# Kernel optimization log

Hardware: AMD Instinct MI355X
Metric: run time of the kernel (lower is better)

## Reference

```python
import jax, jax.numpy as jnp
import numpy as np

T, B = 384, 128
IN_DIM, HID, OUT_DIM = 512, 1024, 512


def _lstm_step(h, c, x_t, Wx, Wh, b):
    # x_t: [B, D], h/c: [B, H]; gates order: i, f, g, o
    gates = x_t @ Wx + h @ Wh + b  # [B, 4H]
    i, f, g, o = jnp.split(gates, 4, axis=-1)
    c_new = jax.nn.sigmoid(f) * c + jax.nn.sigmoid(i) * jnp.tanh(g)
    h_new = jax.nn.sigmoid(o) * jnp.tanh(c_new)
    return h_new, c_new


def setup_inputs() -> dict:
    key = jax.random.key(0)
    ks = jax.random.split(key, 9)
    s_in = 1.0 / np.sqrt(IN_DIM)
    s_h = 1.0 / np.sqrt(HID)
    s_o = 1.0 / np.sqrt(OUT_DIM)
    return {
        "x": jax.random.normal(ks[0], (T, B, IN_DIM), dtype=jnp.float32),
        "hidden_state": jnp.zeros((1, B, HID), dtype=jnp.float32),
        "cell_state": jnp.zeros((1, B, HID), dtype=jnp.float32),
        "enc_Wx": jax.random.normal(ks[1], (IN_DIM, 4 * HID), dtype=jnp.float32) * s_in,
        "enc_Wh": jax.random.normal(ks[2], (HID, 4 * HID), dtype=jnp.float32) * s_h,
        "enc_b": jnp.zeros((4 * HID,), dtype=jnp.float32),
        "dec_Wx": jax.random.normal(ks[3], (OUT_DIM, 4 * HID), dtype=jnp.float32) * s_o,
        "dec_Wh": jax.random.normal(ks[4], (HID, 4 * HID), dtype=jnp.float32) * s_h,
        "dec_b": jnp.zeros((4 * HID,), dtype=jnp.float32),
        "fc_W": jax.random.normal(ks[5], (HID, OUT_DIM), dtype=jnp.float32) * s_h,
        "fc_b": jnp.zeros((OUT_DIM,), dtype=jnp.float32),
    }


def reference(x, hidden_state, cell_state, enc_Wx, enc_Wh, enc_b,
              dec_Wx, dec_Wh, dec_b, fc_W, fc_b):
    # ---- encoder: run LSTM over T steps, keep only final hidden state ----
    h0, c0 = hidden_state[0], cell_state[0]  # [B, H]

    def enc_step(carry, x_t):
        h, c = carry
        h, c = _lstm_step(h, c, x_t, enc_Wx, enc_Wh, enc_b)
        return (h, c), None

    (h_enc, _), _ = jax.lax.scan(enc_step, (h0, c0), x)

    y0 = jnp.zeros((B, OUT_DIM), dtype=x.dtype)
    c_dec0 = jnp.zeros((B, HID), dtype=x.dtype)

    def dec_step(carry, _):
        y, h, c = carry
        h, c = _lstm_step(h, c, y, dec_Wx, dec_Wh, dec_b)
        y = jax.nn.softmax(h @ fc_W + fc_b, axis=-1)  # softmax over dim=2
        return (y, h, c), y

    _, output = jax.lax.scan(dec_step, (y0, h_enc, c_dec0), None, length=T)
    return output  # [T, B, OUT_DIM]
```

## Files before the change

### kernel.cpp

```cpp
#include <hip/hip_runtime.h>


#define TS 384

typedef __attribute__((ext_vector_type(8))) short bf16x8;
typedef __attribute__((ext_vector_type(4))) float f32x4;

#define WS_XR 4096u
#define XR_SLOT 262144u
#define WS_HP (WS_XR + 4u*XR_SLOT)
#define HP_BUF 524288u
#define WS_FPN (WS_HP + 2u*HP_BUF)
#define WS_TOTAL (WS_FPN + 2097152u)

__device__ __forceinline__ unsigned short bf16r(float v) {
  unsigned u = __float_as_uint(v);
  u += 0x7FFFu + ((u >> 16) & 1u);
  return (unsigned short)(u >> 16);
}
__device__ __forceinline__ float bf2f(unsigned short h) {
  return __uint_as_float(((unsigned)h) << 16);
}
__device__ __forceinline__ void split2(float v, short& hi, short& lo) {
  unsigned short h = bf16r(v);
  float r = v - bf2f(h);
  hi = (short)h; lo = (short)bf16r(r);
}
__device__ __forceinline__ float sigm(float v)  { return 1.0f / (1.0f + __expf(-v)); }
__device__ __forceinline__ float tanhfa(float v){ return 1.0f - 2.0f / (__expf(2.0f*v) + 1.0f); }

__device__ __forceinline__ void st_u64(short* p, unsigned long long v) {
  __hip_atomic_store((unsigned long long*)p, v, __ATOMIC_RELAXED, __HIP_MEMORY_SCOPE_AGENT);
}
__device__ __forceinline__ void st_f32(float* p, float v) {
  __hip_atomic_store(p, v, __ATOMIC_RELAXED, __HIP_MEMORY_SCOPE_AGENT);
}
__device__ __forceinline__ float ld_f32(const float* p) {
  return __hip_atomic_load(p, __ATOMIC_RELAXED, __HIP_MEMORY_SCOPE_AGENT);
}
__device__ __forceinline__ unsigned ldc(const unsigned* p) {
  return __hip_atomic_load(p, __ATOMIC_RELAXED, __HIP_MEMORY_SCOPE_AGENT);
}

__device__ __forceinline__ void arrive(unsigned* line) {
  asm volatile("s_waitcnt vmcnt(0)" ::: "memory");
  __syncthreads();
  if (threadIdx.x == 0)
    __hip_atomic_fetch_add(line, 1u, __ATOMIC_RELAXED, __HIP_MEMORY_SCOPE_AGENT);
}
__device__ __forceinline__ void wait4(const unsigned* base, unsigned target,
                                      bool fence, int* sDead) {
  if (threadIdx.x == 0) {
    unsigned spins = 0;
    for (;;) {
      unsigned c0 = ldc(base), c1 = ldc(base + 64);
      unsigned c2 = ldc(base + 128), c3 = ldc(base + 192);
      if (c0 >= target && c1 >= target && c2 >= target && c3 >= target) break;
      __builtin_amdgcn_s_sleep(1);
      if (++spins > (1u << 19)) { *sDead = 1; break; }
    }
    if (fence) __builtin_amdgcn_fence(__ATOMIC_ACQUIRE, "agent");
  }
  __syncthreads();
}
__device__ __forceinline__ void wait1(const unsigned* line, unsigned target,
                                      int* sDead) {
  if (threadIdx.x == 0) {
    unsigned spins = 0;
    while (ldc(line) < target) {
      __builtin_amdgcn_s_sleep(1);
      if (++spins > (1u << 19)) { *sDead = 1; break; }
    }
  }
  __syncthreads();
}

__device__ void load_gate_weights(const float* __restrict__ Wx, const float* __restrict__ Wh,
                                  int p, short* sBh, short* sBl) {
  for (int idx = threadIdx.x; idx < 24576; idx += 1024) {
    int j = idx & 7, l = (idx >> 3) & 63, kb = idx >> 9;
    int k = kb * 32 + ((l >> 4) << 3) + j;
    int c = l & 15;
    int gcol = (c >> 2) * 1024 + p * 4 + (c & 3);
    float wv = (k < 512) ? Wx[(size_t)k * 4096 + gcol]
                         : Wh[(size_t)(k - 512) * 4096 + gcol];
    short hi, lo; split2(wv, hi, lo);
    sBh[idx] = hi; sBl[idx] = lo;
  }
}
__device__ void load_fc_weights(const float* __restrict__ fcW, int kg, int cg,
                                short* sFh, short* sFl) {
  for (int idx = threadIdx.x; idx < 4096; idx += 1024) {
    int j = idx & 7, l = (idx >> 3) & 63, kb = idx >> 9;
    int unit = kg * 256 + kb * 32 + ((l >> 4) << 3) + j;
    int col = cg * 16 + (l & 15);
    short hi, lo; split2(fcW[(size_t)unit * 512 + col], hi, lo);
    sFh[idx] = hi; sFl[idx] = lo;
  }
}

__device__ __forceinline__ void gg(const short* AHs, const short* ALs,
    const short* BHs, const short* BLs, int mt, int l,
    int kbA0, int kbB0, int nkb, f32x4* acc)
{
  const bf16x8* AH = (const bf16x8*)AHs;
  const bf16x8* AL = (const bf16x8*)ALs;
  const bf16x8* BH = (const bf16x8*)BHs;
  const bf16x8* BL = (const bf16x8*)BLs;
  #pragma unroll 2
  for (int i = 0; i < nkb; i += 2) {
    int ka = kbA0 + i, kb = kbB0 + i;
    bf16x8 ah0 = AH[(ka * 8 + mt) * 64 + l];
    bf16x8 al0 = AL[(ka * 8 + mt) * 64 + l];
    bf16x8 bh0 = BH[kb * 64 + l];
    bf16x8 bl0 = BL[kb * 64 + l];
    bf16x8 ah1 = AH[((ka + 1) * 8 + mt) * 64 + l];
    bf16x8 al1 = AL[((ka + 1) * 8 + mt) * 64 + l];
    bf16x8 bh1 = BH[(kb + 1) * 64 + l];
    bf16x8 bl1 = BL[(kb + 1) * 64 + l];
    acc[0] = __builtin_amdgcn_mfma_f32_16x16x32_bf16(ah0, bh0, acc[0], 0, 0, 0);
    acc[1] = __builtin_amdgcn_mfma_f32_16x16x32_bf16(ah0, bl0, acc[1], 0, 0, 0);
    acc[2] = __builtin_amdgcn_mfma_f32_16x16x32_bf16(al0, bh0, acc[2], 0, 0, 0);
    acc[3] = __builtin_amdgcn_mfma_f32_16x16x32_bf16(ah1, bh1, acc[3], 0, 0, 0);
    acc[4] = __builtin_amdgcn_mfma_f32_16x16x32_bf16(ah1, bl1, acc[4], 0, 0, 0);
    acc[5] = __builtin_amdgcn_mfma_f32_16x16x32_bf16(al1, bh1, acc[5], 0, 0, 0);
  }
}
__device__ __forceinline__ void gg_finish(f32x4* acc, int kh, int mt, int l,
                                          float* LDSgate) {
  f32x4 s = (acc[0] + acc[3]) + ((acc[1] + acc[4]) + (acc[2] + acc[5]));
  const int col = l & 15, r0 = mt * 16 + ((l >> 4) << 2);
  float* plane = LDSgate + kh * 2176;
  #pragma unroll
  for (int j = 0; j < 4; ++j) plane[(r0 + j) * 17 + col] = s[j];
}

__device__ __forceinline__ void conv_x(const float* __restrict__ xsrc,
                                       short* dstH, short* dstL, int p, int t) {
  if (t < 32) {
    int g = p * 32 + t;
    int l = g & 63, mt = (g >> 6) & 7, kb = g >> 9;
    int row = mt * 16 + (l & 15), k = kb * 32 + ((l >> 4) << 3);
    const float* xs = xsrc + (size_t)row * 512 + k;
    unsigned long long h64[2] = {0, 0}, l64[2] = {0, 0};
    #pragma unroll
    for (int j = 0; j < 8; ++j) {
      short hi, lo; split2(xs[j], hi, lo);
      h64[j >> 2] |= (unsigned long long)(unsigned short)hi << ((j & 3) * 16);
      l64[j >> 2] |= (unsigned long long)(unsigned short)lo << ((j & 3) * 16);
    }
    int off = g * 8;
    st_u64(dstH + off, h64[0]); st_u64(dstH + off + 4, h64[1]);
    st_u64(dstL + off, l64[0]); st_u64(dstL + off + 4, l64[1]);
  }
}

__global__ void __launch_bounds__(1024, 1)
lstm4(const float* __restrict__ x, const float* __restrict__ h0p,
      const float* __restrict__ c0p, const float* __restrict__ eWx,
      const float* __restrict__ eWh, const float* __restrict__ eb,
      const float* __restrict__ dWx, const float* __restrict__ dWh,
      const float* __restrict__ db, const float* __restrict__ fcW,
      const float* __restrict__ fcb, float* __restrict__ out,
      char* __restrict__ ws)
{
  __shared__ __align__(16) short sBh[24576], sBl[24576];
  __shared__ __align__(16) short sFh[4096], sFl[4096];
  __shared__ float LDSgate[2 * 2176];
  __shared__ unsigned hsplit[512];
  __shared__ float ybuf[512];
  __shared__ float red[16];
  __shared__ int sDead;

  const int p = blockIdx.x, t = threadIdx.x;
  const int w = t >> 6, l = t & 63;
  const int mt = w & 7, kh = w >> 3;
  if (t == 0) sDead = 0;

  unsigned* hln = (unsigned*)ws;
  unsigned* yln = (unsigned*)(ws + 1024);
  unsigned* fln = (unsigned*)(ws + 2048);
  unsigned* my_hline = hln + (p >> 6) * 64;

  short* xrH[4]; short* xrL[4];
  #pragma unroll
  for (int s4 = 0; s4 < 4; ++s4) {
    xrH[s4] = (short*)(ws + WS_XR + s4 * XR_SLOT);
    xrL[s4] = (short*)(ws + WS_XR + s4 * XR_SLOT + 131072u);
  }
  short* hpH[2]; short* hpL[2];
  #pragma unroll
  for (int b2 = 0; b2 < 2; ++b2) {
    hpH[b2] = (short*)(ws + WS_HP + b2 * HP_BUF);
    hpL[b2] = (short*)(ws + WS_HP + b2 * HP_BUF + 262144u);
  }
  float* fp = (float*)(ws + WS_FPN);

  const int row_pw = t & 127, u_pw = (t >> 7) & 3;

  load_gate_weights(eWx, eWh, p, sBh, sBl);
  conv_x(x, xrH[0], xrL[0], p, t);
  conv_x(x + 65536, xrH[1], xrL[1], p, t);
  if (t < 64) {
    int hg = p * 64 + t;
    int ll = hg & 63, mtt = (hg >> 6) & 7, hk = hg >> 9;
    int row = mtt * 16 + (ll & 15), k = hk * 32 + ((ll >> 4) << 3);
    const float* hs = h0p + (size_t)row * 1024 + k;
    unsigned long long h64[2] = {0, 0}, l64[2] = {0, 0};
    #pragma unroll
    for (int j = 0; j < 8; ++j) {
      short hi, lo; split2(hs[j], hi, lo);
      h64[j >> 2] |= (unsigned long long)(unsigned short)hi << ((j & 3) * 16);
      l64[j >> 2] |= (unsigned long long)(unsigned short)lo << ((j & 3) * 16);
    }
    int off = hg * 8;
    st_u64(hpH[0] + off, h64[0]); st_u64(hpH[0] + off + 4, h64[1]);
    st_u64(hpL[0] + off, l64[0]); st_u64(hpL[0] + off + 4, l64[1]);
  }
  float creg = 0.f, bq0 = 0.f, bq1 = 0.f, bq2 = 0.f, bq3 = 0.f;
  if (t < 512) {
    creg = c0p[(size_t)row_pw * 1024 + p * 4 + u_pw];
    bq0 = eb[0 * 1024 + p * 4 + u_pw];
    bq1 = eb[1 * 1024 + p * 4 + u_pw];
    bq2 = eb[2 * 1024 + p * 4 + u_pw];
    bq3 = eb[3 * 1024 + p * 4 + u_pw];
  }
  arrive(my_hline);
  wait4(hln, 64u, true, &sDead);
  if (sDead) return;

  for (int st = 0; st < TS; ++st) {
    int rb = st & 1, wb = rb ^ 1, xs = st & 3;
    f32x4 z = {0.f, 0.f, 0.f, 0.f};
    f32x4 acc[6] = {z, z, z, z, z, z};
    gg(xrH[xs], xrL[xs], sBh, sBl, mt, l, kh * 8, kh * 8, 8, acc);
    wait4(hln, 64u * (st + 1), true, &sDead);
    if (sDead) return;
    gg(hpH[rb], hpL[rb], sBh, sBl, mt, l, kh * 16, 16 + kh * 16, 16, acc);
    gg_finish(acc, kh, mt, l, LDSgate);
    __syncthreads();
    if (t < 512) {
      float g0 = LDSgate[row_pw * 17 + 0  + u_pw] + LDSgate[2176 + row_pw * 17 + 0  + u_pw] + bq0;
      float g1 = LDSgate[row_pw * 17 + 4  + u_pw] + LDSgate[2176 + row_pw * 17 + 4  + u_pw] + bq1;
      float g2 = LDSgate[row_pw * 17 + 8  + u_pw] + LDSgate[2176 + row_pw * 17 + 8  + u_pw] + bq2;
      float g3 = LDSgate[row_pw * 17 + 12 + u_pw] + LDSgate[2176 + row_pw * 17 + 12 + u_pw] + bq3;
      creg = sigm(g1) * creg + sigm(g0) * tanhfa(g2);
      float h = sigm(g3) * tanhfa(creg);
      short hi, lo; split2(h, hi, lo);
      hsplit[u_pw * 128 + row_pw] = ((unsigned)(unsigned short)hi << 16) | (unsigned short)lo;
    }
    if (st + 2 < TS)
      conv_x(x + (size_t)(st + 2) * 65536, xrH[(st + 2) & 3], xrL[(st + 2) & 3], p, t);
    __syncthreads();
    if (t < 128) {
      int r = t;
      unsigned w0 = hsplit[r], w1 = hsplit[128 + r], w2 = hsplit[256 + r], w3 = hsplit[384 + r];
      unsigned long long hi64 = (unsigned long long)(w0 >> 16)
        | ((unsigned long long)(w1 >> 16) << 16)
        | ((unsigned long long)(w2 >> 16) << 32)
        | ((unsigned long long)(w3 >> 16) << 48);
      unsigned long long lo64 = (unsigned long long)(w0 & 0xFFFFu)
        | ((unsigned long long)(w1 & 0xFFFFu) << 16)
        | ((unsigned long long)(w2 & 0xFFFFu) << 32)
        | ((unsigned long long)(w3 & 0xFFFFu) << 48);
      int hk = p >> 3, mtt = r >> 4;
      int lane_ = (((p >> 1) & 3) << 4) | (r & 15);
      int off = ((hk * 8 + mtt) * 64 + lane_) * 8 + (p & 1) * 4;
      st_u64(hpH[wb] + off, hi64);
      st_u64(hpL[wb] + off, lo64);
    }
    arrive(my_hline);
  }

  load_gate_weights(dWx, dWh, p, sBh, sBl);
  if (p >= 128) load_fc_weights(fcW, (p - 128) >> 5, (p - 128) & 31, sFh, sFl);
  if (t < 32) {
    int off = (p * 32 + t) * 8;
    st_u64(xrH[0] + off, 0ull); st_u64(xrH[0] + off + 4, 0ull);
    st_u64(xrL[0] + off, 0ull); st_u64(xrL[0] + off + 4, 0ull);
  }
  creg = 0.0f;
  if (t < 512) {
    bq0 = db[0 * 1024 + p * 4 + u_pw];
    bq1 = db[1 * 1024 + p * 4 + u_pw];
    bq2 = db[2 * 1024 + p * 4 + u_pw];
    bq3 = db[3 * 1024 + p * 4 + u_pw];
  }
  float fcb_r = (t < 512) ? fcb[t] : 0.f;
  arrive(my_hline);

  const unsigned HB = (unsigned)(TS + 2);
  for (int st = 0; st < TS; ++st) {
    int rb = st & 1, wb = rb ^ 1;
    int ys = st & 1, yw = ys ^ 1;
    f32x4 z = {0.f, 0.f, 0.f, 0.f};
    f32x4 acc[6] = {z, z, z, z, z, z};
    wait4(hln, 64u * (HB + st), true, &sDead);
    if (sDead) return;
    gg(hpH[rb], hpL[rb], sBh, sBl, mt, l, kh * 16, 16 + kh * 16, 16, acc);
    wait4(yln, 32u * st, false, &sDead);
    if (sDead) return;
    gg(xrH[ys], xrL[ys], sBh, sBl, mt, l, kh * 8, kh * 8, 8, acc);
    gg_finish(acc, kh, mt, l, LDSgate);
    __syncthreads();
    if (t < 512) {
      float g0 = LDSgate[row_pw * 17 + 0  + u_pw] + LDSgate[2176 + row_pw * 17 + 0  + u_pw] + bq0;
      float g1 = LDSgate[row_pw * 17 + 4  + u_pw] + LDSgate[2176 + row_pw * 17 + 4  + u_pw] + bq1;
      float g2 = LDSgate[row_pw * 17 + 8  + u_pw] + LDSgate[2176 + row_pw * 17 + 8  + u_pw] + bq2;
      float g3 = LDSgate[row_pw * 17 + 12 + u_pw] + LDSgate[2176 + row_pw * 17 + 12 + u_pw] + bq3;
      creg = sigm(g1) * creg + sigm(g0) * tanhfa(g2);
      float h = sigm(g3) * tanhfa(creg);
      short hi, lo; split2(h, hi, lo);
      hsplit[u_pw * 128 + row_pw] = ((unsigned)(unsigned short)hi << 16) | (unsigned short)lo;
    }
    __syncthreads();
    if (t < 128) {
      int r = t;
      unsigned w0 = hsplit[r], w1 = hsplit[128 + r], w2 = hsplit[256 + r], w3 = hsplit[384 + r];
      unsigned long long hi64 = (unsigned long long)(w0 >> 16)
        | ((unsigned long long)(w1 >> 16) << 16)
        | ((unsigned long long)(w2 >> 16) << 32)
        | ((unsigned long long)(w3 >> 16) << 48);
      unsigned long long lo64 = (unsigned long long)(w0 & 0xFFFFu)
        | ((unsigned long long)(w1 & 0xFFFFu) << 16)
        | ((unsigned long long)(w2 & 0xFFFFu) << 32)
        | ((unsigned long long)(w3 & 0xFFFFu) << 48);
      int hk = p >> 3, mtt = r >> 4;
      int lane_ = (((p >> 1) & 3) << 4) | (r & 15);
      int off = ((hk * 8 + mtt) * 64 + lane_) * 8 + (p & 1) * 4;
      st_u64(hpH[wb] + off, hi64);
      st_u64(hpL[wb] + off, lo64);
    }
    arrive(my_hline);

    if (p >= 128) {
      const int f = p - 128, kg = f >> 5, cg = f & 31;
      wait1(hln + kg * 64, 64u * (HB + st + 1), &sDead);
      if (sDead) return;
      {
        const bf16x8* AH = (const bf16x8*)hpH[wb];
        const bf16x8* AL = (const bf16x8*)hpL[wb];
        const bf16x8* BH = (const bf16x8*)sFh;
        const bf16x8* BL = (const bf16x8*)sFl;
        f32x4 a0 = z, a1 = z, a2 = z;
        #pragma unroll
        for (int kb = 0; kb < 4; ++kb) {
          int hk = kg * 8 + kh * 4 + kb;
          bf16x8 ah = AH[(hk * 8 + mt) * 64 + l];
          bf16x8 al = AL[(hk * 8 + mt) * 64 + l];
          bf16x8 bh = BH[(kh * 4 + kb) * 64 + l];
          bf16x8 bl = BL[(kh * 4 + kb) * 64 + l];
          a0 = __builtin_amdgcn_mfma_f32_16x16x32_bf16(ah, bh, a0, 0, 0, 0);
          a1 = __builtin_amdgcn_mfma_f32_16x16x32_bf16(ah, bl, a1, 0, 0, 0);
          a2 = __builtin_amdgcn_mfma_f32_16x16x32_bf16(al, bh, a2, 0, 0, 0);
        }
        f32x4 s = a0 + (a1 + a2);
        int slice = kg * 2 + kh;
        int col = cg * 16 + (l & 15), r0 = mt * 16 + ((l >> 4) << 2);
        #pragma unroll
        for (int j = 0; j < 4; ++j)
          st_f32(&fp[(size_t)(slice * 128 + r0 + j) * 512 + col], s[j]);
      }
      arrive(fln + (f >> 5) * 64);
    } else {
      wait4(fln, 32u * (st + 1), false, &sDead);
      if (sDead) return;
      float v = 0.f, e = 0.f, mx;
      if (t < 512) {
        v = fcb_r;
        #pragma unroll
        for (int s8 = 0; s8 < 8; ++s8)
          v += ld_f32(&fp[(size_t)(s8 * 128 + p) * 512 + t]);
        mx = v;
        #pragma unroll
        for (int o = 32; o > 0; o >>= 1) mx = fmaxf(mx, __shfl_xor(mx, o));
        if (l == 0) red[w] = mx;
      }
      __syncthreads();
      if (t < 512) {
        mx = red[0];
        #pragma unroll
        for (int i = 1; i < 8; ++i) mx = fmaxf(mx, red[i]);
        e = __expf(v - mx);
        float ss = e;
        #pragma unroll
        for (int o = 32; o > 0; o >>= 1) ss += __shfl_xor(ss, o);
        if (l == 0) red[8 + w] = ss;
      }
      __syncthreads();
      if (t < 512) {
        float ss = (red[8] + red[9]) + (red[10] + red[11])
                 + (red[12] + red[13]) + (red[14] + red[15]);
        float y = e / ss;
        out[((size_t)st * 128 + p) * 512 + t] = y;
        ybuf[t] = y;
      }
      __syncthreads();
      if (t < 64) {
        int kb = t >> 2, seg = t & 3;
        int k = kb * 32 + seg * 8;
        int lane_ = (seg << 4) | (p & 15), mtt = p >> 4;
        int off = ((kb * 8 + mtt) * 64 + lane_) * 8;
        unsigned long long h64[2] = {0, 0}, l64[2] = {0, 0};
        #pragma unroll
        for (int j = 0; j < 8; ++j) {
          short hi, lo; split2(ybuf[k + j], hi, lo);
          h64[j >> 2] |= (unsigned long long)(unsigned short)hi << ((j & 3) * 16);
          l64[j >> 2] |= (unsigned long long)(unsigned short)lo << ((j & 3) * 16);
        }
        st_u64(xrH[yw] + off, h64[0]); st_u64(xrH[yw] + off + 4, h64[1]);
        st_u64(xrL[yw] + off, l64[0]); st_u64(xrL[yw] + off + 4, l64[1]);
      }
      arrive(yln + (p >> 5) * 64);
    }
  }
}

extern "C" void kernel_launch(void* const* d_in, const int* in_sizes, int n_in,
                              void* d_out, int out_size, void* d_ws, size_t ws_size,
                              hipStream_t stream) {
  const float* x   = (const float*)d_in[0];
  const float* h0  = (const float*)d_in[1];
  const float* c0  = (const float*)d_in[2];
  const float* eWx = (const float*)d_in[3];
  const float* eWh = (const float*)d_in[4];
  const float* eb  = (const float*)d_in[5];
  const float* dWx = (const float*)d_in[6];
  const float* dWh = (const float*)d_in[7];
  const float* db  = (const float*)d_in[8];
  const float* fcW = (const float*)d_in[9];
  const float* fcb = (const float*)d_in[10];
  float* out = (float*)d_out;

  if (ws_size < (size_t)WS_TOTAL) {
    hipMemsetAsync(d_out, 0xFF, (size_t)out_size * sizeof(float), stream);
    return;
  }
  hipMemsetAsync(d_ws, 0, 4096, stream);
  hipLaunchKernelGGL(lstm4, dim3(256), dim3(1024), 0, stream,
                     x, h0, c0, eWx, eWh, eb, dWx, dWh, db, fcW, fcb, out,
                     (char*)d_ws);
}
```

Measured before the change: 14.97 ms.

## Split gate GEMM across K-slices per block group with workspace partial-sum reduction

Changes the work split of the persistent LSTM kernel. Each block used to compute full-K gates for 16 columns. Now groups of 8 blocks share 32 gate columns, and each block handles one K-slice: x for encoder or y for decoder on k<4, h on k>=4. Partial results go to a global workspace and are reduced after a per-group barrier. The encoder x GEMM now reads and splits fp32 x directly, which drops the staged conversion buffers, and the x/y work no longer waits on the h barrier. This overlaps the input projection with the recurrence but adds a second global barrier and more global traffic per step.

```diff
diff --git a/kernel.cpp b/kernel.cpp
--- a/kernel.cpp
+++ b/kernel.cpp
@@ -2,16 +2,16 @@
 
 
 #define TS 384
+#define DBASE (TS + 2)
 
 typedef __attribute__((ext_vector_type(8))) short bf16x8;
 typedef __attribute__((ext_vector_type(4))) float f32x4;
 
-#define WS_XR 4096u
-#define XR_SLOT 262144u
-#define WS_HP (WS_XR + 4u*XR_SLOT)
-#define HP_BUF 524288u
-#define WS_FPN (WS_HP + 2u*HP_BUF)
-#define WS_TOTAL (WS_FPN + 2097152u)
+#define WS_C   8192u
+#define WS_HP  16785408u
+#define WS_YP  17833984u
+#define WS_FPD 18096128u
+#define WS_TOTAL 20193280u
 
 __device__ __forceinline__ unsigned short bf16r(float v) {
   unsigned u = __float_as_uint(v);
@@ -29,7 +29,7 @@
 __device__ __forceinline__ float sigm(float v)  { return 1.0f / (1.0f + __expf(-v)); }
 __device__ __forceinline__ float tanhfa(float v){ return 1.0f - 2.0f / (__expf(2.0f*v) + 1.0f); }
 
-__device__ __forceinline__ void st_u64(short* p, unsigned long long v) {
+__device__ __forceinline__ void st_u64(void* p, unsigned long long v) {
   __hip_atomic_store((unsigned long long*)p, v, __ATOMIC_RELAXED, __HIP_MEMORY_SCOPE_AGENT);
 }
 __device__ __forceinline__ void st_f32(float* p, float v) {
@@ -40,6 +40,13 @@
 }
 __device__ __forceinline__ unsigned ldc(const unsigned* p) {
   return __hip_atomic_load(p, __ATOMIC_RELAXED, __HIP_MEMORY_SCOPE_AGENT);
+}
+union FRAG { unsigned long long q[2]; bf16x8 v; };
+__device__ __forceinline__ bf16x8 ld_frag(const short* base) {
+  FRAG u;
+  u.q[0] = __hip_atomic_load((const unsigned long long*)base, __ATOMIC_RELAXED, __HIP_MEMORY_SCOPE_AGENT);
+  u.q[1] = __hip_atomic_load((const unsigned long long*)(base + 4), __ATOMIC_RELAXED, __HIP_MEMORY_SCOPE_AGENT);
+  return u.v;
 }
 
 __device__ __forceinline__ void arrive(unsigned* line) {
@@ -48,8 +55,7 @@
   if (threadIdx.x == 0)
     __hip_atomic_fetch_add(line, 1u, __ATOMIC_RELAXED, __HIP_MEMORY_SCOPE_AGENT);
 }
-__device__ __forceinline__ void wait4(const unsigned* base, unsigned target,
-                                      bool fence, int* sDead) {
+__device__ __forceinline__ void wait4(const unsigned* base, unsigned target, int* sDead) {
   if (threadIdx.x == 0) {
     unsigned spins = 0;
     for (;;) {
@@ -59,12 +65,10 @@
       __builtin_amdgcn_s_sleep(1);
       if (++spins > (1u << 19)) { *sDead = 1; break; }
     }
-    if (fence) __builtin_amdgcn_fence(__ATOMIC_ACQUIRE, "agent");
   }
   __syncthreads();
 }
-__device__ __forceinline__ void wait1(const unsigned* line, unsigned target,
-                                      int* sDead) {
+__device__ __forceinline__ void wait1(const unsigned* line, unsigned target, int* sDead) {
   if (threadIdx.x == 0) {
     unsigned spins = 0;
     while (ldc(line) < target) {
@@ -75,21 +79,30 @@
   __syncthreads();
 }
 
-__device__ void load_gate_weights(const float* __restrict__ Wx, const float* __restrict__ Wh,
-                                  int p, short* sBh, short* sBl) {
-  for (int idx = threadIdx.x; idx < 24576; idx += 1024) {
-    int j = idx & 7, l = (idx >> 3) & 63, kb = idx >> 9;
-    int k = kb * 32 + ((l >> 4) << 3) + j;
-    int c = l & 15;
-    int gcol = (c >> 2) * 1024 + p * 4 + (c & 3);
-    float wv = (k < 512) ? Wx[(size_t)k * 4096 + gcol]
-                         : Wh[(size_t)(k - 512) * 4096 + gcol];
-    short hi, lo; split2(wv, hi, lo);
-    sBh[idx] = hi; sBl[idx] = lo;
-  }
-}
-__device__ void load_fc_weights(const float* __restrict__ fcW, int kg, int cg,
-                                short* sFh, short* sFl) {
+__device__ void load_gw(const float* __restrict__ Wx, const float* __restrict__ Wh,
+                        int n, int k, short* sBh, short* sBl) {
+  if (k < 4) {
+    for (int idx = threadIdx.x; idx < 16384; idx += 1024) {
+      int j = idx & 7, l = (idx >> 3) & 63, kb = (idx >> 9) & 3, nt = idx >> 11;
+      int K = k * 128 + kb * 32 + ((l >> 4) << 3) + j;
+      int c = nt * 16 + (l & 15);
+      int gcol = ((c >> 2) & 3) * 1024 + n * 32 + ((c >> 4) << 2) + (c & 3);
+      short hi, lo; split2(Wx[(size_t)K * 4096 + gcol], hi, lo);
+      sBh[idx] = hi; sBl[idx] = lo;
+    }
+  } else {
+    for (int idx = threadIdx.x; idx < 32768; idx += 1024) {
+      int j = idx & 7, l = (idx >> 3) & 63, kb = (idx >> 9) & 7, nt = idx >> 12;
+      int K = (k - 4) * 256 + kb * 32 + ((l >> 4) << 3) + j;
+      int c = nt * 16 + (l & 15);
+      int gcol = ((c >> 2) & 3) * 1024 + n * 32 + ((c >> 4) << 2) + (c & 3);
+      short hi, lo; split2(Wh[(size_t)K * 4096 + gcol], hi, lo);
+      sBh[idx] = hi; sBl[idx] = lo;
+    }
+  }
+}
+__device__ void load_fcw(const float* __restrict__ fcW, int kg, int cg,
+                         short* sFh, short* sFl) {
   for (int idx = threadIdx.x; idx < 4096; idx += 1024) {
     int j = idx & 7, l = (idx >> 3) & 63, kb = idx >> 9;
     int unit = kg * 256 + kb * 32 + ((l >> 4) << 3) + j;
@@ -99,64 +112,119 @@
   }
 }
 
-__device__ __forceinline__ void gg(const short* AHs, const short* ALs,
-    const short* BHs, const short* BLs, int mt, int l,
-    int kbA0, int kbB0, int nkb, f32x4* acc)
+#define MFMA __builtin_amdgcn_mfma_f32_16x16x32_bf16
+
+__device__ __forceinline__ void gemm_h(const short* hpHc, const short* hpLc,
+    const short* sBh, const short* sBl, int hs, int mt, int nh, int l, f32x4* acc)
 {
-  const bf16x8* AH = (const bf16x8*)AHs;
-  const bf16x8* AL = (const bf16x8*)ALs;
-  const bf16x8* BH = (const bf16x8*)BHs;
-  const bf16x8* BL = (const bf16x8*)BLs;
-  #pragma unroll 2
-  for (int i = 0; i < nkb; i += 2) {
-    int ka = kbA0 + i, kb = kbB0 + i;
-    bf16x8 ah0 = AH[(ka * 8 + mt) * 64 + l];
-    bf16x8 al0 = AL[(ka * 8 + mt) * 64 + l];
-    bf16x8 bh0 = BH[kb * 64 + l];
-    bf16x8 bl0 = BL[kb * 64 + l];
-    bf16x8 ah1 = AH[((ka + 1) * 8 + mt) * 64 + l];
-    bf16x8 al1 = AL[((ka + 1) * 8 + mt) * 64 + l];
-    bf16x8 bh1 = BH[(kb + 1) * 64 + l];
-    bf16x8 bl1 = BL[(kb + 1) * 64 + l];
-    acc[0] = __builtin_amdgcn_mfma_f32_16x16x32_bf16(ah0, bh0, acc[0], 0, 0, 0);
-    acc[1] = __builtin_amdgcn_mfma_f32_16x16x32_bf16(ah0, bl0, acc[1], 0, 0, 0);
-    acc[2] = __builtin_amdgcn_mfma_f32_16x16x32_bf16(al0, bh0, acc[2], 0, 0, 0);
-    acc[3] = __builtin_amdgcn_mfma_f32_16x16x32_bf16(ah1, bh1, acc[3], 0, 0, 0);
-    acc[4] = __builtin_amdgcn_mfma_f32_16x16x32_bf16(ah1, bl1, acc[4], 0, 0, 0);
-    acc[5] = __builtin_amdgcn_mfma_f32_16x16x32_bf16(al1, bh1, acc[5], 0, 0, 0);
-  }
-}
-__device__ __forceinline__ void gg_finish(f32x4* acc, int kh, int mt, int l,
-                                          float* LDSgate) {
-  f32x4 s = (acc[0] + acc[3]) + ((acc[1] + acc[4]) + (acc[2] + acc[5]));
-  const int col = l & 15, r0 = mt * 16 + ((l >> 4) << 2);
-  float* plane = LDSgate + kh * 2176;
+  const bf16x8* BH = (const bf16x8*)sBh;
+  const bf16x8* BL = (const bf16x8*)sBl;
+  const int kb0 = hs * 8;
+  bf16x8 ah = ld_frag(hpHc + ((kb0 * 8 + mt) * 64 + l) * 8);
+  bf16x8 al = ld_frag(hpLc + ((kb0 * 8 + mt) * 64 + l) * 8);
   #pragma unroll
-  for (int j = 0; j < 4; ++j) plane[(r0 + j) * 17 + col] = s[j];
-}
-
-__device__ __forceinline__ void conv_x(const float* __restrict__ xsrc,
-                                       short* dstH, short* dstL, int p, int t) {
-  if (t < 32) {
-    int g = p * 32 + t;
-    int l = g & 63, mt = (g >> 6) & 7, kb = g >> 9;
-    int row = mt * 16 + (l & 15), k = kb * 32 + ((l >> 4) << 3);
-    const float* xs = xsrc + (size_t)row * 512 + k;
-    unsigned long long h64[2] = {0, 0}, l64[2] = {0, 0};
-    #pragma unroll
-    for (int j = 0; j < 8; ++j) {
-      short hi, lo; split2(xs[j], hi, lo);
-      h64[j >> 2] |= (unsigned long long)(unsigned short)hi << ((j & 3) * 16);
-      l64[j >> 2] |= (unsigned long long)(unsigned short)lo << ((j & 3) * 16);
-    }
-    int off = g * 8;
-    st_u64(dstH + off, h64[0]); st_u64(dstH + off + 4, h64[1]);
-    st_u64(dstL + off, l64[0]); st_u64(dstL + off + 4, l64[1]);
+  for (int kb = 0; kb < 8; ++kb) {
+    bf16x8 ahn = ah, aln = al;
+    if (kb < 7) {
+      ahn = ld_frag(hpHc + (((kb0 + kb + 1) * 8 + mt) * 64 + l) * 8);
+      aln = ld_frag(hpLc + (((kb0 + kb + 1) * 8 + mt) * 64 + l) * 8);
+    }
+    bf16x8 bh[4], bl[4];
+    #pragma unroll
+    for (int i = 0; i < 4; ++i) {
+      bh[i] = BH[((nh * 4 + i) * 8 + kb) * 64 + l];
+      bl[i] = BL[((nh * 4 + i) * 8 + kb) * 64 + l];
+    }
+    #pragma unroll
+    for (int i = 0; i < 4; ++i) acc[i] = MFMA(ah, bh[i], acc[i], 0, 0, 0);
+    #pragma unroll
+    for (int i = 0; i < 4; ++i) acc[i] = MFMA(ah, bl[i], acc[i], 0, 0, 0);
+    #pragma unroll
+    for (int i = 0; i < 4; ++i) acc[i] = MFMA(al, bh[i], acc[i], 0, 0, 0);
+    ah = ahn; al = aln;
+  }
+}
+
+__device__ __forceinline__ void gemm_x_enc(const float* __restrict__ xsrc,
+    const short* sBh, const short* sBl, int xs, int mt, int nh, int l, f32x4* acc)
+{
+  const bf16x8* BH = (const bf16x8*)sBh;
+  const bf16x8* BL = (const bf16x8*)sBl;
+  const int row = mt * 16 + (l & 15);
+  #pragma unroll
+  for (int kb = 0; kb < 4; ++kb) {
+    const int kc = (xs * 4 + kb) * 32 + ((l >> 4) << 3);
+    const float* xp = xsrc + (size_t)row * 512 + kc;
+    float4 f0 = *(const float4*)xp;
+    float4 f1 = *(const float4*)(xp + 4);
+    union { bf16x8 v; short s[8]; } Ah, Al;
+    split2(f0.x, Ah.s[0], Al.s[0]); split2(f0.y, Ah.s[1], Al.s[1]);
+    split2(f0.z, Ah.s[2], Al.s[2]); split2(f0.w, Ah.s[3], Al.s[3]);
+    split2(f1.x, Ah.s[4], Al.s[4]); split2(f1.y, Ah.s[5], Al.s[5]);
+    split2(f1.z, Ah.s[6], Al.s[6]); split2(f1.w, Ah.s[7], Al.s[7]);
+    bf16x8 bh[4], bl[4];
+    #pragma unroll
+    for (int i = 0; i < 4; ++i) {
+      bh[i] = BH[((nh * 4 + i) * 4 + kb) * 64 + l];
+      bl[i] = BL[((nh * 4 + i) * 4 + kb) * 64 + l];
+    }
+    #pragma unroll
+    for (int i = 0; i < 4; ++i) acc[i] = MFMA(Ah.v, bh[i], acc[i], 0, 0, 0);
+    #pragma unroll
+    for (int i = 0; i < 4; ++i) acc[i] = MFMA(Ah.v, bl[i], acc[i], 0, 0, 0);
+    #pragma unroll
+    for (int i = 0; i < 4; ++i) acc[i] = MFMA(Al.v, bh[i], acc[i], 0, 0, 0);
+  }
+}
+
+__device__ __forceinline__ void gemm_x_dec(const short* ypH, const short* ypL,
+    const short* sBh, const short* sBl, int xs, int mt, int nh, int l, f32x4* acc)
+{
+  const bf16x8* BH = (const bf16x8*)sBh;
+  const bf16x8* BL = (const bf16x8*)sBl;
+  const int kb0 = xs * 4;
+  bf16x8 ah = ld_frag(ypH + ((kb0 * 8 + mt) * 64 + l) * 8);
+  bf16x8 al = ld_frag(ypL + ((kb0 * 8 + mt) * 64 + l) * 8);
+  #pragma unroll
+  for (int kb = 0; kb < 4; ++kb) {
+    bf16x8 ahn = ah, aln = al;
+    if (kb < 3) {
+      ahn = ld_frag(ypH + (((kb0 + kb + 1) * 8 + mt) * 64 + l) * 8);
+      aln = ld_frag(ypL + (((kb0 + kb + 1) * 8 + mt) * 64 + l) * 8);
+    }
+    bf16x8 bh[4], bl[4];
+    #pragma unroll
+    for (int i = 0; i < 4; ++i) {
+      bh[i] = BH[((nh * 4 + i) * 4 + kb) * 64 + l];
+      bl[i] = BL[((nh * 4 + i) * 4 + kb) * 64 + l];
+    }
+    #pragma unroll
+    for (int i = 0; i < 4; ++i) acc[i] = MFMA(ah, bh[i], acc[i], 0, 0, 0);
+    #pragma unroll
+    for (int i = 0; i < 4; ++i) acc[i] = MFMA(ah, bl[i], acc[i], 0, 0, 0);
+    #pragma unroll
+    for (int i = 0; i < 4; ++i) acc[i] = MFMA(al, bh[i], acc[i], 0, 0, 0);
+    ah = ahn; al = aln;
+  }
+}
+
+__device__ __forceinline__ void store_C(char* ws, int p, int mt, int nh, int l,
+                                        const f32x4* acc) {
+  float* Cm = (float*)(ws + WS_C) + (size_t)p * 16384;
+  const int r0 = mt * 16 + ((l >> 4) << 2);
+  #pragma unroll
+  for (int i = 0; i < 4; ++i) {
+    int col = (nh * 4 + i) * 16 + (l & 15);
+    float* dst = Cm + col * 128 + r0;
+    union { float f[2]; unsigned long long q; } a, b;
+    a.f[0] = acc[i][0]; a.f[1] = acc[i][1];
+    b.f[0] = acc[i][2]; b.f[1] = acc[i][3];
+    st_u64(dst, a.q); st_u64(dst + 2, b.q);
   }
 }
 
 __global__ void __launch_bounds__(1024, 1)
-lstm4(const float* __restrict__ x, const float* __restrict__ h0p,
+lstm5(const float* __restrict__ x, const float* __restrict__ h0p,
       const float* __restrict__ c0p, const float* __restrict__ eWx,
       const float* __restrict__ eWh, const float* __restrict__ eb,
       const float* __restrict__ dWx, const float* __restrict__ dWh,
@@ -164,9 +232,8 @@
       const float* __restrict__ fcb, float* __restrict__ out,
       char* __restrict__ ws)
 {
-  __shared__ __align__(16) short sBh[24576], sBl[24576];
+  __shared__ __align__(16) short sBh[32768], sBl[32768];
   __shared__ __align__(16) short sFh[4096], sFl[4096];
-  __shared__ float LDSgate[2 * 2176];
   __shared__ unsigned hsplit[512];
   __shared__ float ybuf[512];
   __shared__ float red[16];
@@ -174,38 +241,35 @@
 
   const int p = blockIdx.x, t = threadIdx.x;
   const int w = t >> 6, l = t & 63;
-  const int mt = w & 7, kh = w >> 3;
+  const int mt = w & 7, nh = w >> 3;
+  const int n = p >> 3, k = p & 7;
   if (t == 0) sDead = 0;
 
-  unsigned* hln = (unsigned*)ws;
-  unsigned* yln = (unsigned*)(ws + 1024);
-  unsigned* fln = (unsigned*)(ws + 2048);
+  unsigned* hln  = (unsigned*)ws;
+  unsigned* pln  = (unsigned*)(ws + 1024) + n * 32;
+  unsigned* flnB = (unsigned*)(ws + 5376);
+  unsigned* ylnB = (unsigned*)(ws + 6400);
   unsigned* my_hline = hln + (p >> 6) * 64;
 
-  short* xrH[4]; short* xrL[4];
-  #pragma unroll
-  for (int s4 = 0; s4 < 4; ++s4) {
-    xrH[s4] = (short*)(ws + WS_XR + s4 * XR_SLOT);
-    xrL[s4] = (short*)(ws + WS_XR + s4 * XR_SLOT + 131072u);
-  }
   short* hpH[2]; short* hpL[2];
   #pragma unroll
   for (int b2 = 0; b2 < 2; ++b2) {
-    hpH[b2] = (short*)(ws + WS_HP + b2 * HP_BUF);
-    hpL[b2] = (short*)(ws + WS_HP + b2 * HP_BUF + 262144u);
-  }
-  float* fp = (float*)(ws + WS_FPN);
+    hpH[b2] = (short*)(ws + WS_HP + b2 * 524288u);
+    hpL[b2] = (short*)(ws + WS_HP + b2 * 524288u + 262144u);
+  }
+  short* ypH = (short*)(ws + WS_YP);
+  short* ypL = (short*)(ws + WS_YP + 131072u);
+  float* fp  = (float*)(ws + WS_FPD);
+  const float* Cgrp = (const float*)(ws + WS_C) + (size_t)(n * 8) * 16384;
 
   const int row_pw = t & 127, u_pw = (t >> 7) & 3;
 
-  load_gate_weights(eWx, eWh, p, sBh, sBl);
-  conv_x(x, xrH[0], xrL[0], p, t);
-  conv_x(x + 65536, xrH[1], xrL[1], p, t);
+  load_gw(eWx, eWh, n, k, sBh, sBl);
   if (t < 64) {
     int hg = p * 64 + t;
     int ll = hg & 63, mtt = (hg >> 6) & 7, hk = hg >> 9;
-    int row = mtt * 16 + (ll & 15), k = hk * 32 + ((ll >> 4) << 3);
-    const float* hs = h0p + (size_t)row * 1024 + k;
+    int row = mtt * 16 + (ll & 15), kcol = hk * 32 + ((ll >> 4) << 3);
+    const float* hs = h0p + (size_t)row * 1024 + kcol;
     unsigned long long h64[2] = {0, 0}, l64[2] = {0, 0};
     #pragma unroll
     for (int j = 0; j < 8; ++j) {
@@ -213,9 +277,8 @@
       h64[j >> 2] |= (unsigned long long)(unsigned short)hi << ((j & 3) * 16);
       l64[j >> 2] |= (unsigned long long)(unsigned short)lo << ((j & 3) * 16);
     }
-    int off = hg * 8;
-    st_u64(hpH[0] + off, h64[0]); st_u64(hpH[0] + off + 4, h64[1]);
-    st_u64(hpL[0] + off, l64[0]); st_u64(hpL[0] + off + 4, l64[1]);
+    st_u64(hpH[0] + hg * 8, h64[0]); st_u64(hpH[0] + hg * 8 + 4, h64[1]);
+    st_u64(hpL[0] + hg * 8, l64[0]); st_u64(hpL[0] + hg * 8 + 4, l64[1]);
   }
   float creg = 0.f, bq0 = 0.f, bq1 = 0.f, bq2 = 0.f, bq3 = 0.f;
   if (t < 512) {
@@ -226,31 +289,42 @@
     bq3 = eb[3 * 1024 + p * 4 + u_pw];
   }
   arrive(my_hline);
-  wait4(hln, 64u, true, &sDead);
-  if (sDead) return;
 
   for (int st = 0; st < TS; ++st) {
-    int rb = st & 1, wb = rb ^ 1, xs = st & 3;
+    const int rp = st & 1, wp = rp ^ 1;
     f32x4 z = {0.f, 0.f, 0.f, 0.f};
-    f32x4 acc[6] = {z, z, z, z, z, z};
-    gg(xrH[xs], xrL[xs], sBh, sBl, mt, l, kh * 8, kh * 8, 8, acc);
-    wait4(hln, 64u * (st + 1), true, &sDead);
+    f32x4 acc[4] = {z, z, z, z};
+    if (k < 4) {
+      gemm_x_enc(x + (size_t)st * 65536, sBh, sBl, k, mt, nh, l, acc);
+      wait4(hln, 64u * (st + 1), &sDead);
+      if (sDead) return;
+    } else {
+      wait4(hln, 64u * (st + 1), &sDead);
+      if (sDead) return;
+      gemm_h(hpH[rp], hpL[rp], sBh, sBl, k - 4, mt, nh, l, acc);
+    }
+    store_C(ws, p, mt, nh, l, acc);
+    arrive(pln);
+    wait1(pln, 8u * (st + 1), &sDead);
     if (sDead) return;
-    gg(hpH[rb], hpL[rb], sBh, sBl, mt, l, kh * 16, 16 + kh * 16, 16, acc);
-    gg_finish(acc, kh, mt, l, LDSgate);
-    __syncthreads();
     if (t < 512) {
-      float g0 = LDSgate[row_pw * 17 + 0  + u_pw] + LDSgate[2176 + row_pw * 17 + 0  + u_pw] + bq0;
-      float g1 = LDSgate[row_pw * 17 + 4  + u_pw] + LDSgate[2176 + row_pw * 17 + 4  + u_pw] + bq1;
-      float g2 = LDSgate[row_pw * 17 + 8  + u_pw] + LDSgate[2176 + row_pw * 17 + 8  + u_pw] + bq2;
-      float g3 = LDSgate[row_pw * 17 + 12 + u_pw] + LDSgate[2176 + row_pw * 17 + 12 + u_pw] + bq3;
+      const int cb = (k * 16 + u_pw) * 128 + row_pw;
+      float v[32];
+      #pragma unroll
+      for (int sb = 0; sb < 8; ++sb)
+        #pragma unroll
+        for (int q = 0; q < 4; ++q)
+          v[sb * 4 + q] = ld_f32(Cgrp + sb * 16384 + q * 512 + cb);
+      float g0 = bq0, g1 = bq1, g2 = bq2, g3 = bq3;
+      #pragma unroll
+      for (int sb = 0; sb < 8; ++sb) {
+        g0 += v[sb * 4]; g1 += v[sb * 4 + 1]; g2 += v[sb * 4 + 2]; g3 += v[sb * 4 + 3];
+      }
       creg = sigm(g1) * creg + sigm(g0) * tanhfa(g2);
       float h = sigm(g3) * tanhfa(creg);
       short hi, lo; split2(h, hi, lo);
       hsplit[u_pw * 128 + row_pw] = ((unsigned)(unsigned short)hi << 16) | (unsigned short)lo;
     }
-    if (st + 2 < TS)
-      conv_x(x + (size_t)(st + 2) * 65536, xrH[(st + 2) & 3], xrL[(st + 2) & 3], p, t);
     __syncthreads();
     if (t < 128) {
       int r = t;
@@ -266,18 +340,24 @@
       int hk = p >> 3, mtt = r >> 4;
       int lane_ = (((p >> 1) & 3) << 4) | (r & 15);
       int off = ((hk * 8 + mtt) * 64 + lane_) * 8 + (p & 1) * 4;
-      st_u64(hpH[wb] + off, hi64);
-      st_u64(hpL[wb] + off, lo64);
+      st_u64(hpH[wp] + off, hi64);
+      st_u64(hpL[wp] + off, lo64);
     }
     arrive(my_hline);
   }
 
-  load_gate_weights(dWx, dWh, p, sBh, sBl);
-  if (p >= 128) load_fc_weights(fcW, (p - 128) >> 5, (p - 128) & 31, sFh, sFl);
-  if (t < 32) {
-    int off = (p * 32 + t) * 8;
-    st_u64(xrH[0] + off, 0ull); st_u64(xrH[0] + off + 4, 0ull);
-    st_u64(xrL[0] + off, 0ull); st_u64(xrL[0] + off + 4, 0ull);
+  load_gw(dWx, dWh, n, k, sBh, sBl);
+  int kg = 0, cg = 0, row_sm = 0;
+  if (k >= 4) {
+    int f = n * 4 + (k - 4); kg = f >> 5; cg = f & 31;
+    load_fcw(fcW, kg, cg, sFh, sFl);
+  } else {
+    row_sm = n * 4 + k;
+  }
+  if (t < 64) {
+    int i64 = p * 64 + t;
+    st_u64(ypH + i64 * 4, 0ull);
+    st_u64(ypL + i64 * 4, 0ull);
   }
   creg = 0.0f;
   if (t < 512) {
@@ -289,25 +369,37 @@
   float fcb_r = (t < 512) ? fcb[t] : 0.f;
   arrive(my_hline);
 
-  const unsigned HB = (unsigned)(TS + 2);
   for (int st = 0; st < TS; ++st) {
-    int rb = st & 1, wb = rb ^ 1;
-    int ys = st & 1, yw = ys ^ 1;
+    const int rp = st & 1, wp = rp ^ 1;
     f32x4 z = {0.f, 0.f, 0.f, 0.f};
-    f32x4 acc[6] = {z, z, z, z, z, z};
-    wait4(hln, 64u * (HB + st), true, &sDead);
+    f32x4 acc[4] = {z, z, z, z};
+    if (k >= 4) {
+      wait4(hln, 64u * (DBASE + st), &sDead);
+      if (sDead) return;
+      gemm_h(hpH[rp], hpL[rp], sBh, sBl, k - 4, mt, nh, l, acc);
+    } else {
+      if (st == 0) { wait4(hln, 64u * DBASE, &sDead); if (sDead) return; }
+      wait4(ylnB, 32u * st, &sDead);
+      if (sDead) return;
+      gemm_x_dec(ypH, ypL, sBh, sBl, k, mt, nh, l, acc);
+    }
+    store_C(ws, p, mt, nh, l, acc);
+    arrive(pln);
+    wait1(pln, 8u * (TS + st + 1), &sDead);
     if (sDead) return;
-    gg(hpH[rb], hpL[rb], sBh, sBl, mt, l, kh * 16, 16 + kh * 16, 16, acc);
-    wait4(yln, 32u * st, false, &sDead);
-    if (sDead) return;
-    gg(xrH[ys], xrL[ys], sBh, sBl, mt, l, kh * 8, kh * 8, 8, acc);
-    gg_finish(acc, kh, mt, l, LDSgate);
-    __syncthreads();
     if (t < 512) {
-      float g0 = LDSgate[row_pw * 17 + 0  + u_pw] + LDSgate[2176 + row_pw * 17 + 0  + u_pw] + bq0;
-      float g1 = LDSgate[row_pw * 17 + 4  + u_pw] + LDSgate[2176 + row_pw * 17 + 4  + u_pw] + bq1;
-      float g2 = LDSgate[row_pw * 17 + 8  + u_pw] + LDSgate[2176 + row_pw * 17 + 8  + u_pw] + bq2;
-      float g3 = LDSgate[row_pw * 17 + 12 + u_pw] + LDSgate[2176 + row_pw * 17 + 12 + u_pw] + bq3;
+      const int cb = (k * 16 + u_pw) * 128 + row_pw;
+      float v[32];
+      #pragma unroll
+      for (int sb = 0; sb < 8; ++sb)
+        #pragma unroll
+        for (int q = 0; q < 4; ++q)
+          v[sb * 4 + q] = ld_f32(Cgrp + sb * 16384 + q * 512 + cb);
+      float g0 = bq0, g1 = bq1, g2 = bq2, g3 = bq3;
+      #pragma unroll
+      for (int sb = 0; sb < 8; ++sb) {
+        g0 += v[sb * 4]; g1 += v[sb * 4 + 1]; g2 += v[sb * 4 + 2]; g3 += v[sb * 4 + 3];
+      }
       creg = sigm(g1) * creg + sigm(g0) * tanhfa(g2);
       float h = sigm(g3) * tanhfa(creg);
       short hi, lo; split2(h, hi, lo);
@@ -328,49 +420,46 @@
       int hk = p >> 3, mtt = r >> 4;
       int lane_ = (((p >> 1) & 3) << 4) | (r & 15);
       int off = ((hk * 8 + mtt) * 64 + lane_) * 8 + (p & 1) * 4;
-      st_u64(hpH[wb] + off, hi64);
-      st_u64(hpL[wb] + off, lo64);
+      st_u64(hpH[wp] + off, hi64);
+      st_u64(hpL[wp] + off, lo64);
     }
     arrive(my_hline);
 
-    if (p >= 128) {
-      const int f = p - 128, kg = f >> 5, cg = f & 31;
-      wait1(hln + kg * 64, 64u * (HB + st + 1), &sDead);
+    if (k >= 4) {
+      wait1(hln + kg * 64, 64u * (DBASE + st + 1), &sDead);
       if (sDead) return;
       {
-        const bf16x8* AH = (const bf16x8*)hpH[wb];
-        const bf16x8* AL = (const bf16x8*)hpL[wb];
-        const bf16x8* BH = (const bf16x8*)sFh;
-        const bf16x8* BL = (const bf16x8*)sFl;
+        const bf16x8* FB = (const bf16x8*)sFh;
+        const bf16x8* FL = (const bf16x8*)sFl;
         f32x4 a0 = z, a1 = z, a2 = z;
         #pragma unroll
         for (int kb = 0; kb < 4; ++kb) {
-          int hk = kg * 8 + kh * 4 + kb;
-          bf16x8 ah = AH[(hk * 8 + mt) * 64 + l];
-          bf16x8 al = AL[(hk * 8 + mt) * 64 + l];
-          bf16x8 bh = BH[(kh * 4 + kb) * 64 + l];
-          bf16x8 bl = BL[(kh * 4 + kb) * 64 + l];
-          a0 = __builtin_amdgcn_mfma_f32_16x16x32_bf16(ah, bh, a0, 0, 0, 0);
-          a1 = __builtin_amdgcn_mfma_f32_16x16x32_bf16(ah, bl, a1, 0, 0, 0);
-          a2 = __builtin_amdgcn_mfma_f32_16x16x32_bf16(al, bh, a2, 0, 0, 0);
+          int gkb = kg * 8 + nh * 4 + kb;
+          bf16x8 ah = ld_frag(hpH[wp] + ((gkb * 8 + mt) * 64 + l) * 8);
+          bf16x8 al = ld_frag(hpL[wp] + ((gkb * 8 + mt) * 64 + l) * 8);
+          bf16x8 bh = FB[(nh * 4 + kb) * 64 + l];
+          bf16x8 bl = FL[(nh * 4 + kb) * 64 + l];
+          a0 = MFMA(ah, bh, a0, 0, 0, 0);
+          a1 = MFMA(ah, bl, a1, 0, 0, 0);
+          a2 = MFMA(al, bh, a2, 0, 0, 0);
         }
         f32x4 s = a0 + (a1 + a2);
-        int slice = kg * 2 + kh;
+        int slice = kg * 2 + nh;
         int col = cg * 16 + (l & 15), r0 = mt * 16 + ((l >> 4) << 2);
         #pragma unroll
         for (int j = 0; j < 4; ++j)
           st_f32(&fp[(size_t)(slice * 128 + r0 + j) * 512 + col], s[j]);
       }
-      arrive(fln + (f >> 5) * 64);
+      arrive(flnB + (n >> 3) * 64);
     } else {
-      wait4(fln, 32u * (st + 1), false, &sDead);
+      wait4(flnB, 32u * (st + 1), &sDead);
       if (sDead) return;
       float v = 0.f, e = 0.f, mx;
       if (t < 512) {
         v = fcb_r;
         #pragma unroll
         for (int s8 = 0; s8 < 8; ++s8)
-          v += ld_f32(&fp[(size_t)(s8 * 128 + p) * 512 + t]);
+          v += ld_f32(&fp[(size_t)(s8 * 128 + row_sm) * 512 + t]);
         mx = v;
         #pragma unroll
         for (int o = 32; o > 0; o >>= 1) mx = fmaxf(mx, __shfl_xor(mx, o));
@@ -392,26 +481,26 @@
         float ss = (red[8] + red[9]) + (red[10] + red[11])
                  + (red[12] + red[13]) + (red[14] + red[15]);
         float y = e / ss;
-        out[((size_t)st * 128 + p) * 512 + t] = y;
+        out[((size_t)st * 128 + row_sm) * 512 + t] = y;
         ybuf[t] = y;
       }
       __syncthreads();
       if (t < 64) {
         int kb = t >> 2, seg = t & 3;
-        int k = kb * 32 + seg * 8;
-        int lane_ = (seg << 4) | (p & 15), mtt = p >> 4;
+        int kcol = kb * 32 + seg * 8;
+        int lane_ = (seg << 4) | (row_sm & 15), mtt = row_sm >> 4;
         int off = ((kb * 8 + mtt) * 64 + lane_) * 8;
         unsigned long long h64[2] = {0, 0}, l64[2] = {0, 0};
         #pragma unroll
         for (int j = 0; j < 8; ++j) {
-          short hi, lo; split2(ybuf[k + j], hi, lo);
+          short hi, lo; split2(ybuf[kcol + j], hi, lo);
           h64[j >> 2] |= (unsigned long long)(unsigned short)hi << ((j & 3) * 16);
           l64[j >> 2] |= (unsigned long long)(unsigned short)lo << ((j & 3) * 16);
         }
-        st_u64(xrH[yw] + off, h64[0]); st_u64(xrH[yw] + off + 4, h64[1]);
-        st_u64(xrL[yw] + off, l64[0]); st_u64(xrL[yw] + off + 4, l64[1]);
-      }
-      arrive(yln + (p >> 5) * 64);
+        st_u64(ypH + off, h64[0]); st_u64(ypH + off + 4, h64[1]);
+        st_u64(ypL + off, l64[0]); st_u64(ypL + off + 4, l64[1]);
+      }
+      arrive(ylnB + (n >> 3) * 64);
     }
   }
 }
@@ -436,8 +525,8 @@
     hipMemsetAsync(d_out, 0xFF, (size_t)out_size * sizeof(float), stream);
     return;
   }
-  hipMemsetAsync(d_ws, 0, 4096, stream);
-  hipLaunchKernelGGL(lstm4, dim3(256), dim3(1024), 0, stream,
+  hipMemsetAsync(d_ws, 0, 8192, stream);
+  hipLaunchKernelGGL(lstm5, dim3(256), dim3(1024), 0, stream,
                      x, h0, c0, eWx, eWh, eb, dWx, dWh, db, fcW, fcb, out,
                      (char*)d_ws);
 }
```

Measured after the change: 24.66 ms. 64.7% more time.
